# Optimization experiments

Measured on AMD Instinct MI355X. Metric: run time of the kernel, lower is better.

## Reference

```python
import jax, jax.numpy as jnp
import numpy as np

F, H, NSEQ, T, A, LP, LV = 256, 256, 64, 2048, 32, 512, 512
N = NSEQ * T


def setup_inputs() -> dict:
    key = jax.random.key(0)
    ks = jax.random.split(key, 24)
    p = lambda k, shape: jax.random.normal(k, shape, jnp.float32) * 0.05
    return {
        'features': jax.random.normal(ks[0], (N, F), jnp.float32),
        'episode_starts': (jax.random.uniform(ks[1], (N,)) < 0.005).astype(jnp.float32),
        'h_pi': jax.random.normal(ks[2], (1, NSEQ, H), jnp.float32),
        'c_pi': jax.random.normal(ks[3], (1, NSEQ, H), jnp.float32),
        'h_vf': jax.random.normal(ks[4], (1, NSEQ, H), jnp.float32),
        'c_vf': jax.random.normal(ks[5], (1, NSEQ, H), jnp.float32),
        'W_feat': p(ks[6], (4 * F, F)), 'b_feat': jnp.zeros((4 * F,), jnp.float32),
        'W_emb': p(ks[7], (H, F)), 'b_emb': jnp.zeros((H,), jnp.float32),
        'W_ih': p(ks[8], (4 * H, F)), 'W_hh': p(ks[9], (4 * H, H)),
        'b_ih': jnp.zeros((4 * H,), jnp.float32), 'b_hh': jnp.zeros((4 * H,), jnp.float32),
        'Wp1': p(ks[10], (LP, H + 3 * F)), 'bp1': jnp.zeros((LP,), jnp.float32),
        'Wp2': p(ks[11], (A, LP)), 'bp2': jnp.zeros((A,), jnp.float32),
        'Wv1': p(ks[12], (LV, H + 3 * F)), 'bv1': jnp.zeros((LV,), jnp.float32),
        'Wv2': p(ks[13], (1, LV)), 'bv2': jnp.zeros((1,), jnp.float32),
    }


def _lstm_masked_scan(feats, starts, h0, c0, W_ih, W_hh, b_ih, b_hh):
    # feats: (T, n_seq, F), starts: (T, n_seq); PyTorch gate order i,f,g,o
    xg = jnp.einsum('tnf,gf->tng', feats, W_ih) + b_ih  # precompute input gates

    def step(carry, xs):
        h, c = carry
        xg_t, s_t = xs
        m = (1.0 - s_t)[:, None]          # episode-reset mask
        h = h * m
        c = c * m
        g = xg_t + h @ W_hh.T + b_hh
        i, f, gg, o = jnp.split(g, 4, axis=-1)
        c = jax.nn.sigmoid(f) * c + jax.nn.sigmoid(i) * jnp.tanh(gg)
        h = jax.nn.sigmoid(o) * jnp.tanh(c)
        return (h, c), h

    (hT, cT), hs = jax.lax.scan(step, (h0, c0), (xg, starts))
    return hs, hT, cT


def reference(features, episode_starts, h_pi, c_pi, h_vf, c_vf,
              W_feat, b_feat, W_emb, b_emb, W_ih, W_hh, b_ih, b_hh,
              Wp1, bp1, Wp2, bp2, Wv1, bv1, Wv2, bv2):
    n_seq = h_vf.shape[1]
    feats = features.reshape(n_seq, -1, F).swapaxes(0, 1)      # (T, n_seq, F)
    starts = episode_starts.reshape(n_seq, -1).swapaxes(0, 1)  # (T, n_seq)

    feat4 = jnp.einsum('tnf,gf->tng', feats, W_feat) + b_feat  # (T, n_seq, 4F)
    f1 = feat4[..., : 3 * F]
    f1_flat = f1.swapaxes(0, 1).reshape(-1, 3 * F)             # (N, 3F)

    # actor branch: TempLSTM ignores its LSTM -> just Linear(F, H) on raw feats;
    # the loop branch feeds raw features_sequence (source behavior).
    out_pi = jnp.einsum('tnf,hf->tnh', feats, W_emb) + b_emb   # (T, n_seq, H)
    out_pi_flat = out_pi.swapaxes(0, 1).reshape(-1, H)

    # critic branch: masked LSTM recurrence with per-step episode resets
    hs, hT, cT = _lstm_masked_scan(feats, starts, h_vf[0], c_vf[0], W_ih, W_hh, b_ih, b_hh)
    hs_flat = hs.swapaxes(0, 1).reshape(-1, H)

    latent_pi = jnp.concatenate([f1_flat, out_pi_flat], axis=-1)
    latent_vf = jnp.concatenate([f1_flat, hs_flat], axis=-1)

    values = jax.nn.relu(latent_vf @ Wv1.T + bv1) @ Wv2.T + bv2      # (N, 1)
    logits = jax.nn.relu(latent_pi @ Wp1.T + bp1) @ Wp2.T + bp2      # (N, A)

    actions = jnp.argmax(logits, axis=-1)  # deterministic=True -> mode
    log_prob = jnp.take_along_axis(jax.nn.log_softmax(logits, axis=-1), actions[:, None], axis=1)[:, 0]

    # actor final state = h0 scaled by product of reset masks (loop semantics)
    mprod = jnp.prod(1.0 - starts, axis=0)[None, :, None]
    h_pi_f, c_pi_f = h_pi * mprod, c_pi * mprod
    return actions, values, log_prob, h_pi_f, c_pi_f, hT[None], cT[None]
```

## Files before the change

kernel.cpp:

```cpp
#include <hip/hip_runtime.h>
#include <stdint.h>
#include <math.h>

#define N_TOT 131072
#define TSEQ  2048
#define NSEQ  64
#define CS    128
#define NCH   16
#define PARTS 4

typedef unsigned long long u64;

__global__ __launch_bounds__(256)
void transpose_whh(const float* __restrict__ Whh, float* __restrict__ Wg)
{
    const int k = blockIdx.x;
    const int u = threadIdx.x;
#pragma unroll
    for (int g = 0; g < 4; ++g)
        Wg[(size_t)k * 1024 + u * 4 + g] = Whh[(size_t)(g * 256 + u) * 256 + k];
}

__global__ __launch_bounds__(256)
void gemm_xg(const float* __restrict__ A, const float* __restrict__ Wih,
             const float* __restrict__ bih, const float* __restrict__ bhh,
             float* __restrict__ xg, int base)
{
    __shared__ float As[16][136];
    __shared__ float Bs[16][136];
    const int t  = threadIdx.x;
    const int n0 = blockIdx.x * 128;
    const int seq = blockIdx.y;
    const size_t grow0 = (size_t)seq * TSEQ + base;
    const size_t lrow0 = (size_t)seq * CS;
    const int tx = t & 15, ty = t >> 4;

    float acc[8][8];
#pragma unroll
    for (int i = 0; i < 8; ++i)
#pragma unroll
        for (int j = 0; j < 8; ++j) acc[i][j] = 0.f;

    for (int kt = 0; kt < 256; kt += 16) {
#pragma unroll
        for (int jj = 0; jj < 2; ++jj) {
            int idx = t + 256 * jj;
            int m = idx >> 2, q = idx & 3;
            float4 a = *(const float4*)(A + (grow0 + m) * 256 + kt + q * 4);
            As[q * 4 + 0][m] = a.x; As[q * 4 + 1][m] = a.y;
            As[q * 4 + 2][m] = a.z; As[q * 4 + 3][m] = a.w;
            float4 b = *(const float4*)(Wih + (size_t)(n0 + m) * 256 + kt + q * 4);
            Bs[q * 4 + 0][m] = b.x; Bs[q * 4 + 1][m] = b.y;
            Bs[q * 4 + 2][m] = b.z; Bs[q * 4 + 3][m] = b.w;
        }
        __syncthreads();
#pragma unroll
        for (int k = 0; k < 16; ++k) {
            float4 a0 = *(const float4*)&As[k][ty * 8];
            float4 a1 = *(const float4*)&As[k][ty * 8 + 4];
            float4 b0 = *(const float4*)&Bs[k][tx * 8];
            float4 b1 = *(const float4*)&Bs[k][tx * 8 + 4];
            float av[8] = {a0.x, a0.y, a0.z, a0.w, a1.x, a1.y, a1.z, a1.w};
            float bv[8] = {b0.x, b0.y, b0.z, b0.w, b1.x, b1.y, b1.z, b1.w};
#pragma unroll
            for (int i = 0; i < 8; ++i)
#pragma unroll
                for (int j = 0; j < 8; ++j) acc[i][j] += av[i] * bv[j];
        }
        __syncthreads();
    }
#pragma unroll
    for (int i = 0; i < 8; ++i) {
        size_t lr = lrow0 + ty * 8 + i;
#pragma unroll
        for (int j = 0; j < 8; ++j) {
            int n = n0 + tx * 8 + j;
            int gate = n >> 8, u = n & 255;
            xg[lr * 1024 + u * 4 + gate] = acc[i][j] + bih[n] + bhh[n];
        }
    }
}

__device__ __forceinline__ void l2_store_u64(u64* p, u64 v)
{
    asm volatile("global_store_dwordx2 %0, %1, off"
                 :: "v"(p), "v"(v) : "memory");
}

__device__ __forceinline__ u64 l2_load_u64(const u64* p)
{
    u64 v;
    asm volatile("global_load_dwordx2 %0, %1, off sc0\n\t"
                 "s_waitcnt vmcnt(0)"
                 : "=v"(v) : "v"(p) : "memory");
    return v;
}

__global__ __launch_bounds__(1024)
void lstm4_h1p(const float* __restrict__ xg, const float* __restrict__ starts,
               const float* __restrict__ h0g, const float* __restrict__ c0g,
               float* __restrict__ hstate, float* __restrict__ cstate,
               const float* __restrict__ Wg,
               float* __restrict__ hs, float* __restrict__ hT,
               float* __restrict__ cT,
               u64* __restrict__ hx, u64* __restrict__ hx2,
               unsigned* __restrict__ fastState,
               const float* __restrict__ lat, const float* __restrict__ Wp1,
               const float* __restrict__ bp1, float* __restrict__ h1,
               int base, int fastflag)
{
    __shared__ float smem[9216];

    const int t   = threadIdx.x;
    const int bid = blockIdx.x;

    if (bid < 256) {
        float* hmask = smem;
        float* part  = smem + 256;

        const int slot = bid >> 3;
        const int seq  = (bid & 7) + 8 * (slot >> 2);
        const int p    = slot & 3;
        const int u    = t & 63;
        const int q    = t >> 6;

        float4 Wr[16];
#pragma unroll
        for (int kk = 0; kk < 16; ++kk)
            Wr[kk] = *(const float4*)(Wg + (size_t)(q * 16 + kk) * 1024 + (p * 64 + u) * 4);

        float c_reg = 0.f;
        if (t < 64) {
            const float* csrc = (base == 0) ? c0g : cstate;
            c_reg = csrc[(size_t)seq * 256 + p * 64 + t];
        }

        bool useFast = (fastflag != 0);
        if (useFast) {
            unsigned st = __hip_atomic_load(fastState, __ATOMIC_RELAXED,
                                            __HIP_MEMORY_SCOPE_AGENT);
            if (st != 0u) useFast = false;
        }

        for (int lt = 0; lt < CS; ++lt) {
            const int S = base + lt;
            const float m = 1.f - starts[(size_t)seq * TSEQ + S];

            float4 x4 = make_float4(0.f, 0.f, 0.f, 0.f);
            if (t < 64)
                x4 = *(const float4*)(xg + ((size_t)seq * CS + lt) * 1024 + (p * 64 + t) * 4);

            if (lt == 0) {
                if (t < 256) {
                    const float* hsrc = (base == 0) ? h0g : hstate;
                    hmask[t] = hsrc[(size_t)seq * 256 + t] * m;
                }
            } else {
                if (t < 256) {
                    const size_t idx = (size_t)(S & 1) * (NSEQ * 256) + (size_t)seq * 256 + t;
                    u64 w = 0;
                    if (useFast) {
                        int tries = 0;
                        for (;;) {
                            w = l2_load_u64(&hx2[idx]);
                            if ((unsigned)(w >> 32) == (unsigned)S) break;
                            if (++tries > 768) {
                                useFast = false;
                                __hip_atomic_store(fastState, 1u, __ATOMIC_RELAXED,
                                                   __HIP_MEMORY_SCOPE_AGENT);
                                break;
                            }
                        }
                    }
                    if (!useFast) {
                        unsigned spins = 0;
                        for (;;) {
                            w = __hip_atomic_load(&hx[idx], __ATOMIC_RELAXED,
                                                  __HIP_MEMORY_SCOPE_AGENT);
                            if ((unsigned)(w >> 32) == (unsigned)S) break;
                            __builtin_amdgcn_s_sleep(1);
                            if (++spins > (1u << 18)) break;
                        }
                    }
                    hmask[t] = __uint_as_float((unsigned)w) * m;
                }
            }
            __syncthreads();

            const float* hp = &hmask[q * 16];
            float4 h0 = *(const float4*)(hp + 0);
            float4 h1v_ = *(const float4*)(hp + 4);
            float4 h2 = *(const float4*)(hp + 8);
            float4 h3 = *(const float4*)(hp + 12);
            float hv[16] = {h0.x,h0.y,h0.z,h0.w, h1v_.x,h1v_.y,h1v_.z,h1v_.w,
                            h2.x,h2.y,h2.z,h2.w, h3.x,h3.y,h3.z,h3.w};
            float a0 = 0.f, a1 = 0.f, a2 = 0.f, a3 = 0.f;
#pragma unroll
            for (int kk = 0; kk < 16; ++kk) {
                a0 += hv[kk] * Wr[kk].x;
                a1 += hv[kk] * Wr[kk].y;
                a2 += hv[kk] * Wr[kk].z;
                a3 += hv[kk] * Wr[kk].w;
            }
            *(float4*)&part[(q * 64 + u) * 4] = make_float4(a0, a1, a2, a3);
            __syncthreads();

            if (t < 64) {
                float gi = 0.f, gf = 0.f, gg = 0.f, go = 0.f;
#pragma unroll
                for (int qq = 0; qq < 16; ++qq) {
                    float4 pp = *(const float4*)&part[(qq * 64 + t) * 4];
                    gi += pp.x; gf += pp.y; gg += pp.z; go += pp.w;
                }
                gi += x4.x; gf += x4.y; gg += x4.z; go += x4.w;
                float c = c_reg * m;
                float si = 1.f / (1.f + expf(-gi));
                float sf = 1.f / (1.f + expf(-gf));
                float so = 1.f / (1.f + expf(-go));
                c = sf * c + si * tanhf(gg);
                float h = so * tanhf(c);
                c_reg = c;

                const int gu = p * 64 + t;
                const size_t widx = (size_t)((S + 1) & 1) * (NSEQ * 256)
                                  + (size_t)seq * 256 + gu;
                const u64 pkt = ((u64)(unsigned)(S + 1) << 32)
                              | (u64)__float_as_uint(h);
                if (fastflag) l2_store_u64(&hx2[widx], pkt);
                __hip_atomic_store(&hx[widx], pkt,
                                   __ATOMIC_RELAXED, __HIP_MEMORY_SCOPE_AGENT);
                hs[((size_t)seq * CS + lt) * 256 + gu] = h;
                if (lt == CS - 1) {
                    cstate[(size_t)seq * 256 + gu] = c;
                    hstate[(size_t)seq * 256 + gu] = h;
                }
                if (S == TSEQ - 1) {
                    cT[(size_t)seq * 256 + gu] = c;
                    hT[(size_t)seq * 256 + gu] = h;
                }
            }
        }
    } else {
        const int s    = t >> 8;
        const int t2   = t & 255;
        const int tile = (bid - 256) * 4 + s;
        const int n0   = (tile & 7) * 64;
        const size_t lr0 = (size_t)(tile >> 3) * 64;
        float* As = smem + s * 2304;
        float* Bs = As + 1152;
        const int tx = t2 & 15, ty = t2 >> 4;

        double acc[4][4];
#pragma unroll
        for (int i = 0; i < 4; ++i)
#pragma unroll
            for (int j = 0; j < 4; ++j) acc[i][j] = 0.0;

        for (int kt = 0; kt < 1024; kt += 16) {
            {
                int m = t2 >> 2, q = t2 & 3;
                float4 a = *(const float4*)(lat + (lr0 + m) * 1024 + kt + q * 4);
                As[(q * 4 + 0) * 72 + m] = a.x; As[(q * 4 + 1) * 72 + m] = a.y;
                As[(q * 4 + 2) * 72 + m] = a.z; As[(q * 4 + 3) * 72 + m] = a.w;
                float4 b = *(const float4*)(Wp1 + (size_t)(n0 + m) * 1024 + kt + q * 4);
                Bs[(q * 4 + 0) * 72 + m] = b.x; Bs[(q * 4 + 1) * 72 + m] = b.y;
                Bs[(q * 4 + 2) * 72 + m] = b.z; Bs[(q * 4 + 3) * 72 + m] = b.w;
            }
            __syncthreads();
            float p[4][4];
#pragma unroll
            for (int i = 0; i < 4; ++i)
#pragma unroll
                for (int j = 0; j < 4; ++j) p[i][j] = 0.f;
#pragma unroll
            for (int k = 0; k < 16; ++k) {
                float4 a0 = *(const float4*)&As[k * 72 + ty * 4];
                float4 b0 = *(const float4*)&Bs[k * 72 + tx * 4];
                float av[4] = {a0.x, a0.y, a0.z, a0.w};
                float bv[4] = {b0.x, b0.y, b0.z, b0.w};
#pragma unroll
                for (int i = 0; i < 4; ++i)
#pragma unroll
                    for (int j = 0; j < 4; ++j) p[i][j] += av[i] * bv[j];
            }
#pragma unroll
            for (int i = 0; i < 4; ++i)
#pragma unroll
                for (int j = 0; j < 4; ++j) acc[i][j] += (double)p[i][j];
            __syncthreads();
        }
#pragma unroll
        for (int i = 0; i < 4; ++i) {
            size_t lr = lr0 + ty * 4 + i;
#pragma unroll
            for (int j = 0; j < 4; ++j) {
                int n = n0 + tx * 4 + j;
                float v = (float)acc[i][j] + bp1[n];
                h1[lr * 512 + n] = v > 0.f ? v : 0.f;
            }
        }
    }
}

__global__ __launch_bounds__(256)
void gemm_latent(const float* __restrict__ A, const float* __restrict__ Wfeat,
                 const float* __restrict__ Wemb, const float* __restrict__ bfeat,
                 const float* __restrict__ bemb, float* __restrict__ lat, int base)
{
    __shared__ float As[16][136];
    __shared__ float Bs[16][136];
    const int t  = threadIdx.x;
    const int n0 = blockIdx.x * 128;
    const size_t lr0 = (size_t)blockIdx.y * 128;
    const size_t grow0 = (lr0 >> 7) * TSEQ + base;
    const int tx = t & 15, ty = t >> 4;

    double acc[8][8];
#pragma unroll
    for (int i = 0; i < 8; ++i)
#pragma unroll
        for (int j = 0; j < 8; ++j) acc[i][j] = 0.0;

    for (int kt = 0; kt < 256; kt += 16) {
#pragma unroll
        for (int jj = 0; jj < 2; ++jj) {
            int idx = t + 256 * jj;
            int m = idx >> 2, q = idx & 3;
            float4 a = *(const float4*)(A + (grow0 + m) * 256 + kt + q * 4);
            As[q * 4 + 0][m] = a.x; As[q * 4 + 1][m] = a.y;
            As[q * 4 + 2][m] = a.z; As[q * 4 + 3][m] = a.w;
            int n = n0 + m;
            const float* Brow = (n < 768) ? (Wfeat + (size_t)n * 256)
                                          : (Wemb + (size_t)(n - 768) * 256);
            float4 b = *(const float4*)(Brow + kt + q * 4);
            Bs[q * 4 + 0][m] = b.x; Bs[q * 4 + 1][m] = b.y;
            Bs[q * 4 + 2][m] = b.z; Bs[q * 4 + 3][m] = b.w;
        }
        __syncthreads();
        float p[8][8];
#pragma unroll
        for (int i = 0; i < 8; ++i)
#pragma unroll
            for (int j = 0; j < 8; ++j) p[i][j] = 0.f;
#pragma unroll
        for (int k = 0; k < 16; ++k) {
            float4 a0 = *(const float4*)&As[k][ty * 8];
            float4 a1 = *(const float4*)&As[k][ty * 8 + 4];
            float4 b0 = *(const float4*)&Bs[k][tx * 8];
            float4 b1 = *(const float4*)&Bs[k][tx * 8 + 4];
            float av[8] = {a0.x, a0.y, a0.z, a0.w, a1.x, a1.y, a1.z, a1.w};
            float bv[8] = {b0.x, b0.y, b0.z, b0.w, b1.x, b1.y, b1.z, b1.w};
#pragma unroll
            for (int i = 0; i < 8; ++i)
#pragma unroll
                for (int j = 0; j < 8; ++j) p[i][j] += av[i] * bv[j];
        }
#pragma unroll
        for (int i = 0; i < 8; ++i)
#pragma unroll
            for (int j = 0; j < 8; ++j) acc[i][j] += (double)p[i][j];
        __syncthreads();
    }
#pragma unroll
    for (int i = 0; i < 8; ++i) {
        size_t lr = lr0 + ty * 8 + i;
#pragma unroll
        for (int j = 0; j < 8; ++j) {
            int n = n0 + tx * 8 + j;
            float v = (float)acc[i][j];
            v += (n < 768) ? bfeat[n] : bemb[n - 768];
            lat[lr * 1024 + n] = v;
        }
    }
}

__global__ __launch_bounds__(256)
void gemm_h1v(const float* __restrict__ lat, const float* __restrict__ hs,
              const float* __restrict__ Wv1, const float* __restrict__ bv1,
              float* __restrict__ h1)
{
    __shared__ float As[16][136];
    __shared__ float Bs[16][136];
    const int t  = threadIdx.x;
    const int n0 = blockIdx.x * 128;
    const size_t lrow0 = (size_t)blockIdx.y * 128;
    const int tx = t & 15, ty = t >> 4;

    float acc[8][8];
#pragma unroll
    for (int i = 0; i < 8; ++i)
#pragma unroll
        for (int j = 0; j < 8; ++j) acc[i][j] = 0.f;

    for (int pass = 0; pass < 2; ++pass) {
        const float* A  = (pass == 0) ? lat : hs;
        const int lda   = (pass == 0) ? 1024 : 256;
        const int kmax  = (pass == 0) ? 768 : 256;
        const int boff  = (pass == 0) ? 0 : 768;
        for (int kt = 0; kt < kmax; kt += 16) {
#pragma unroll
            for (int jj = 0; jj < 2; ++jj) {
                int idx = t + 256 * jj;
                int m = idx >> 2, q = idx & 3;
                float4 a = *(const float4*)(A + (lrow0 + m) * lda + kt + q * 4);
                As[q * 4 + 0][m] = a.x; As[q * 4 + 1][m] = a.y;
                As[q * 4 + 2][m] = a.z; As[q * 4 + 3][m] = a.w;
                float4 b = *(const float4*)(Wv1 + (size_t)(n0 + m) * 1024 + boff + kt + q * 4);
                Bs[q * 4 + 0][m] = b.x; Bs[q * 4 + 1][m] = b.y;
                Bs[q * 4 + 2][m] = b.z; Bs[q * 4 + 3][m] = b.w;
            }
            __syncthreads();
#pragma unroll
            for (int k = 0; k < 16; ++k) {
                float4 a0 = *(const float4*)&As[k][ty * 8];
                float4 a1 = *(const float4*)&As[k][ty * 8 + 4];
                float4 b0 = *(const float4*)&Bs[k][tx * 8];
                float4 b1 = *(const float4*)&Bs[k][tx * 8 + 4];
                float av[8] = {a0.x, a0.y, a0.z, a0.w, a1.x, a1.y, a1.z, a1.w};
                float bv[8] = {b0.x, b0.y, b0.z, b0.w, b1.x, b1.y, b1.z, b1.w};
#pragma unroll
                for (int i = 0; i < 8; ++i)
#pragma unroll
                    for (int j = 0; j < 8; ++j) acc[i][j] += av[i] * bv[j];
            }
            __syncthreads();
        }
    }
#pragma unroll
    for (int i = 0; i < 8; ++i) {
        size_t lr = lrow0 + ty * 8 + i;
#pragma unroll
        for (int j = 0; j < 8; ++j) {
            int n = n0 + tx * 8 + j;
            float v = acc[i][j] + bv1[n];
            h1[lr * 512 + n] = v > 0.f ? v : 0.f;
        }
    }
}

__global__ __launch_bounds__(256)
void mask_kernel(const float* __restrict__ starts, const float* __restrict__ h_pi,
                 const float* __restrict__ c_pi,
                 float* __restrict__ o_hpi, float* __restrict__ o_cpi)
{
    __shared__ float red[256];
    const int n = blockIdx.x, t = threadIdx.x;
    float a = 0.f;
    for (int j = 0; j < 8; ++j)
        a = fmaxf(a, starts[(size_t)n * TSEQ + t * 8 + j]);
    red[t] = a; __syncthreads();
    for (int s = 128; s > 0; s >>= 1) {
        if (t < s) red[t] = fmaxf(red[t], red[t + s]);
        __syncthreads();
    }
    float m = (red[0] > 0.f) ? 0.f : 1.f;
    o_hpi[(size_t)n * 256 + t] = h_pi[(size_t)n * 256 + t] * m;
    o_cpi[(size_t)n * 256 + t] = c_pi[(size_t)n * 256 + t] * m;
}

__global__ __launch_bounds__(256)
void policy_finish(const float* __restrict__ h1p, const float* __restrict__ Wp2,
                   const float* __restrict__ bp2,
                   float* __restrict__ o_actions, float* __restrict__ o_logp,
                   int base)
{
    __shared__ float w2t[512 * 32];
    const int t = threadIdx.x;
    for (int j = 0; j < 64; ++j) {
        int idx = t + 256 * j;
        int k = idx >> 5, c = idx & 31;
        w2t[idx] = Wp2[(size_t)c * 512 + k];
    }
    __syncthreads();

    const int c = t & 31;
    size_t lr = (size_t)blockIdx.x * 8 + (t >> 5);
    size_t grow = (lr >> 7) * TSEQ + base + (lr & 127);
    const float* hrow = h1p + lr * 512;
    double s = 0.0;
    for (int k = 0; k < 512; k += 4) {
        float4 h4 = *(const float4*)(hrow + k);
        s += (double)h4.x * (double)w2t[(k + 0) * 32 + c];
        s += (double)h4.y * (double)w2t[(k + 1) * 32 + c];
        s += (double)h4.z * (double)w2t[(k + 2) * 32 + c];
        s += (double)h4.w * (double)w2t[(k + 3) * 32 + c];
    }
    double logit = s + (double)bp2[c];

    double mv = logit; int mi = c;
#pragma unroll
    for (int off = 16; off >= 1; off >>= 1) {
        double ov = __shfl_xor(mv, off, 32);
        int    oi = __shfl_xor(mi, off, 32);
        if (ov > mv || (ov == mv && oi < mi)) { mv = ov; mi = oi; }
    }
    double se = exp(logit - mv);
#pragma unroll
    for (int off = 16; off >= 1; off >>= 1) se += __shfl_xor(se, off, 32);

    if (c == 0) {
        o_actions[grow] = (float)mi;
        o_logp[grow]    = (float)(-log(se));
    }
}

__global__ __launch_bounds__(256)
void value_finish(const float* __restrict__ h1v, const float* __restrict__ Wv2,
                  const float* __restrict__ bv2, float* __restrict__ o_values,
                  int base)
{
    __shared__ float wv[512];
    const int t = threadIdx.x;
    wv[t] = Wv2[t]; wv[t + 256] = Wv2[t + 256];
    __syncthreads();
    const int q = t & 3;
    size_t lr = (size_t)blockIdx.x * 64 + (t >> 2);
    size_t grow = (lr >> 7) * TSEQ + base + (lr & 127);
    const float* hrow = h1v + lr * 512;
    float s = 0.f;
    for (int k = q * 128; k < q * 128 + 128; k += 4) {
        float4 h4 = *(const float4*)(hrow + k);
        float4 w4 = *(const float4*)&wv[k];
        s += h4.x * w4.x + h4.y * w4.y + h4.z * w4.z + h4.w * w4.w;
    }
    s += __shfl_xor(s, 1, 4);
    s += __shfl_xor(s, 2, 4);
    if (q == 0) o_values[grow] = s + bv2[0];
}

extern "C" void kernel_launch(void* const* d_in, const int* in_sizes, int n_in,
                              void* d_out, int out_size, void* d_ws, size_t ws_size,
                              hipStream_t stream)
{
    const float* features = (const float*)d_in[0];
    const float* starts   = (const float*)d_in[1];
    const float* h_pi     = (const float*)d_in[2];
    const float* c_pi     = (const float*)d_in[3];
    const float* h_vf     = (const float*)d_in[4];
    const float* c_vf     = (const float*)d_in[5];
    const float* W_feat   = (const float*)d_in[6];
    const float* b_feat   = (const float*)d_in[7];
    const float* W_emb    = (const float*)d_in[8];
    const float* b_emb    = (const float*)d_in[9];
    const float* W_ih     = (const float*)d_in[10];
    const float* W_hh     = (const float*)d_in[11];
    const float* b_ih     = (const float*)d_in[12];
    const float* b_hh     = (const float*)d_in[13];
    const float* Wp1      = (const float*)d_in[14];
    const float* bp1      = (const float*)d_in[15];
    const float* Wp2      = (const float*)d_in[16];
    const float* bp2      = (const float*)d_in[17];
    const float* Wv1      = (const float*)d_in[18];
    const float* bv1      = (const float*)d_in[19];
    const float* Wv2      = (const float*)d_in[20];
    const float* bv2      = (const float*)d_in[21];

    float* out = (float*)d_out;
    float* o_actions = out;
    float* o_values  = out + N_TOT;
    float* o_logp    = out + 2 * (size_t)N_TOT;
    float* o_hpi     = out + 3 * (size_t)N_TOT;
    float* o_cpi     = o_hpi + NSEQ * 256;
    float* o_hT      = o_cpi + NSEQ * 256;
    float* o_cT      = o_hT  + NSEQ * 256;

    char* ws = (char*)d_ws;
    const size_t MB = 1024 * 1024;
    float* xg_c  = (float*)(ws);
    float* lat_c = (float*)(ws + 32 * MB);
    float* hs_c  = (float*)(ws + 64 * MB);
    float* h1_c  = (float*)(ws + 72 * MB);
    float* Wg    = (float*)(ws + 88 * MB);
    float* hstate = (float*)(ws + 89 * MB);
    float* cstate = (float*)(ws + 89 * MB + 65536);
    u64*   hx     = (u64*)  (ws + 89 * MB + 131072);
    u64*   hx2    = (u64*)  (ws + 89 * MB + 393216);
    unsigned* fastState = (unsigned*)(ws + 89 * MB + 655360);

    const int fastflag = (ws_size >= 89 * MB + 656 * 1024) ? 1 : 0;
    u64* hx2_eff = fastflag ? hx2 : hx;
    unsigned* fs_eff = fastflag ? fastState : (unsigned*)hx;

    transpose_whh<<<256, 256, 0, stream>>>(W_hh, Wg);

    mask_kernel<<<NSEQ, 256, 0, stream>>>(starts, h_pi, c_pi, o_hpi, o_cpi);

    for (int c = 0; c < NCH; ++c) {
        const int base = c * CS;

        gemm_xg<<<dim3(8, NSEQ), 256, 0, stream>>>(features, W_ih, b_ih, b_hh,
                                                   xg_c, base);
        gemm_latent<<<dim3(8, 64), 256, 0, stream>>>(
            features, W_feat, W_emb, b_feat, b_emb, lat_c, base);

        lstm4_h1p<<<512, 1024, 0, stream>>>(xg_c, starts, h_vf, c_vf,
                                            hstate, cstate, Wg,
                                            hs_c, o_hT, o_cT, hx, hx2_eff,
                                            fs_eff,
                                            lat_c, Wp1, bp1, h1_c,
                                            base, fastflag);

        policy_finish<<<1024, 256, 0, stream>>>(h1_c, Wp2, bp2,
                                                o_actions, o_logp, base);

        gemm_h1v<<<dim3(4, 64), 256, 0, stream>>>(lat_c, hs_c, Wv1, bv1, h1_c);
        value_finish<<<128, 256, 0, stream>>>(h1_c, Wv2, bv2, o_values, base);
    }
}
```

Before: 14.74 ms.

## Overlap next-chunk input GEMMs with LSTM recurrence using double-buffered chunks

Halves the chunk length to 64 timesteps and doubles the chunk count. The input-gate and latent GEMMs for the next chunk now run in extra blocks of the fused LSTM kernel, writing into double-buffered workspace, so the standalone pre-recurrence GEMM launches per chunk go away. The aim is to hide feature-projection work behind the latency-bound sequential recurrence and cut launch count per chunk. The cost is more chunks, and so more per-chunk launches of the finish kernels. The larger grid also risks co-residency problems for the spin-waiting recurrence blocks, and the value-path hidden buffer is aliased onto the current xg buffer.

```diff
diff --git a/kernel.cpp b/kernel.cpp
--- a/kernel.cpp
+++ b/kernel.cpp
@@ -5,8 +5,9 @@
 #define N_TOT 131072
 #define TSEQ  2048
 #define NSEQ  64
-#define CS    128
-#define NCH   16
+#define CS    64
+#define NCH   32
+#define ROWS  (NSEQ * CS)
 #define PARTS 4
 
 typedef unsigned long long u64;
@@ -19,66 +20,6 @@
 #pragma unroll
     for (int g = 0; g < 4; ++g)
         Wg[(size_t)k * 1024 + u * 4 + g] = Whh[(size_t)(g * 256 + u) * 256 + k];
-}
-
-__global__ __launch_bounds__(256)
-void gemm_xg(const float* __restrict__ A, const float* __restrict__ Wih,
-             const float* __restrict__ bih, const float* __restrict__ bhh,
-             float* __restrict__ xg, int base)
-{
-    __shared__ float As[16][136];
-    __shared__ float Bs[16][136];
-    const int t  = threadIdx.x;
-    const int n0 = blockIdx.x * 128;
-    const int seq = blockIdx.y;
-    const size_t grow0 = (size_t)seq * TSEQ + base;
-    const size_t lrow0 = (size_t)seq * CS;
-    const int tx = t & 15, ty = t >> 4;
-
-    float acc[8][8];
-#pragma unroll
-    for (int i = 0; i < 8; ++i)
-#pragma unroll
-        for (int j = 0; j < 8; ++j) acc[i][j] = 0.f;
-
-    for (int kt = 0; kt < 256; kt += 16) {
-#pragma unroll
-        for (int jj = 0; jj < 2; ++jj) {
-            int idx = t + 256 * jj;
-            int m = idx >> 2, q = idx & 3;
-            float4 a = *(const float4*)(A + (grow0 + m) * 256 + kt + q * 4);
-            As[q * 4 + 0][m] = a.x; As[q * 4 + 1][m] = a.y;
-            As[q * 4 + 2][m] = a.z; As[q * 4 + 3][m] = a.w;
-            float4 b = *(const float4*)(Wih + (size_t)(n0 + m) * 256 + kt + q * 4);
-            Bs[q * 4 + 0][m] = b.x; Bs[q * 4 + 1][m] = b.y;
-            Bs[q * 4 + 2][m] = b.z; Bs[q * 4 + 3][m] = b.w;
-        }
-        __syncthreads();
-#pragma unroll
-        for (int k = 0; k < 16; ++k) {
-            float4 a0 = *(const float4*)&As[k][ty * 8];
-            float4 a1 = *(const float4*)&As[k][ty * 8 + 4];
-            float4 b0 = *(const float4*)&Bs[k][tx * 8];
-            float4 b1 = *(const float4*)&Bs[k][tx * 8 + 4];
-            float av[8] = {a0.x, a0.y, a0.z, a0.w, a1.x, a1.y, a1.z, a1.w};
-            float bv[8] = {b0.x, b0.y, b0.z, b0.w, b1.x, b1.y, b1.z, b1.w};
-#pragma unroll
-            for (int i = 0; i < 8; ++i)
-#pragma unroll
-                for (int j = 0; j < 8; ++j) acc[i][j] += av[i] * bv[j];
-        }
-        __syncthreads();
-    }
-#pragma unroll
-    for (int i = 0; i < 8; ++i) {
-        size_t lr = lrow0 + ty * 8 + i;
-#pragma unroll
-        for (int j = 0; j < 8; ++j) {
-            int n = n0 + tx * 8 + j;
-            int gate = n >> 8, u = n & 255;
-            xg[lr * 1024 + u * 4 + gate] = acc[i][j] + bih[n] + bhh[n];
-        }
-    }
 }
 
 __device__ __forceinline__ void l2_store_u64(u64* p, u64 v)
@@ -96,18 +37,136 @@
     return v;
 }
 
-__global__ __launch_bounds__(1024)
-void lstm4_h1p(const float* __restrict__ xg, const float* __restrict__ starts,
-               const float* __restrict__ h0g, const float* __restrict__ c0g,
-               float* __restrict__ hstate, float* __restrict__ cstate,
-               const float* __restrict__ Wg,
-               float* __restrict__ hs, float* __restrict__ hT,
-               float* __restrict__ cT,
-               u64* __restrict__ hx, u64* __restrict__ hx2,
-               unsigned* __restrict__ fastState,
-               const float* __restrict__ lat, const float* __restrict__ Wp1,
-               const float* __restrict__ bp1, float* __restrict__ h1,
-               int base, int fastflag)
+__global__ __launch_bounds__(256)
+void gemm_feat(const float* __restrict__ feats,
+               const float* __restrict__ Wih, const float* __restrict__ bih,
+               const float* __restrict__ bhh, float* __restrict__ xgout,
+               const float* __restrict__ Wfeat, const float* __restrict__ Wemb,
+               const float* __restrict__ bfeat, const float* __restrict__ bemb,
+               float* __restrict__ latout, int base)
+{
+    __shared__ float As[1152];
+    __shared__ float Bs[1152];
+    const int t   = threadIdx.x;
+    const int bid = blockIdx.x;
+    const bool isXg = bid < 1024;
+    const int tile = isXg ? bid : bid - 1024;
+    const int n0   = (tile & 15) * 64;
+    const int seq  = tile >> 4;
+    const size_t grow0 = (size_t)seq * TSEQ + base;
+    const size_t lr0   = (size_t)seq * CS;
+    const int tx = t & 15, ty = t >> 4;
+
+    if (isXg) {
+        float acc[4][4];
+#pragma unroll
+        for (int i = 0; i < 4; ++i)
+#pragma unroll
+            for (int j = 0; j < 4; ++j) acc[i][j] = 0.f;
+        for (int kt = 0; kt < 256; kt += 16) {
+            int m = t >> 2, q = t & 3;
+            float4 a = *(const float4*)(feats + (grow0 + m) * 256 + kt + q * 4);
+            As[(q*4+0)*72+m]=a.x; As[(q*4+1)*72+m]=a.y;
+            As[(q*4+2)*72+m]=a.z; As[(q*4+3)*72+m]=a.w;
+            float4 b = *(const float4*)(Wih + (size_t)(n0 + m) * 256 + kt + q * 4);
+            Bs[(q*4+0)*72+m]=b.x; Bs[(q*4+1)*72+m]=b.y;
+            Bs[(q*4+2)*72+m]=b.z; Bs[(q*4+3)*72+m]=b.w;
+            __syncthreads();
+#pragma unroll
+            for (int k = 0; k < 16; ++k) {
+                float4 a0 = *(const float4*)&As[k*72 + ty*4];
+                float4 b0 = *(const float4*)&Bs[k*72 + tx*4];
+                float av[4] = {a0.x,a0.y,a0.z,a0.w};
+                float bv[4] = {b0.x,b0.y,b0.z,b0.w};
+#pragma unroll
+                for (int i = 0; i < 4; ++i)
+#pragma unroll
+                    for (int j = 0; j < 4; ++j) acc[i][j] += av[i]*bv[j];
+            }
+            __syncthreads();
+        }
+#pragma unroll
+        for (int i = 0; i < 4; ++i) {
+            size_t lr = lr0 + ty*4 + i;
+#pragma unroll
+            for (int j = 0; j < 4; ++j) {
+                int n = n0 + tx*4 + j;
+                int gate = n >> 8, u = n & 255;
+                xgout[lr*1024 + u*4 + gate] = acc[i][j] + bih[n] + bhh[n];
+            }
+        }
+    } else {
+        double acc[4][4];
+#pragma unroll
+        for (int i = 0; i < 4; ++i)
+#pragma unroll
+            for (int j = 0; j < 4; ++j) acc[i][j] = 0.0;
+        for (int kt = 0; kt < 256; kt += 16) {
+            int m = t >> 2, q = t & 3;
+            float4 a = *(const float4*)(feats + (grow0 + m) * 256 + kt + q * 4);
+            As[(q*4+0)*72+m]=a.x; As[(q*4+1)*72+m]=a.y;
+            As[(q*4+2)*72+m]=a.z; As[(q*4+3)*72+m]=a.w;
+            int n = n0 + m;
+            const float* Brow = (n < 768) ? (Wfeat + (size_t)n * 256)
+                                          : (Wemb + (size_t)(n - 768) * 256);
+            float4 b = *(const float4*)(Brow + kt + q * 4);
+            Bs[(q*4+0)*72+m]=b.x; Bs[(q*4+1)*72+m]=b.y;
+            Bs[(q*4+2)*72+m]=b.z; Bs[(q*4+3)*72+m]=b.w;
+            __syncthreads();
+            float p[4][4];
+#pragma unroll
+            for (int i = 0; i < 4; ++i)
+#pragma unroll
+                for (int j = 0; j < 4; ++j) p[i][j] = 0.f;
+#pragma unroll
+            for (int k = 0; k < 16; ++k) {
+                float4 a0 = *(const float4*)&As[k*72 + ty*4];
+                float4 b0 = *(const float4*)&Bs[k*72 + tx*4];
+                float av[4] = {a0.x,a0.y,a0.z,a0.w};
+                float bv[4] = {b0.x,b0.y,b0.z,b0.w};
+#pragma unroll
+                for (int i = 0; i < 4; ++i)
+#pragma unroll
+                    for (int j = 0; j < 4; ++j) p[i][j] += av[i]*bv[j];
+            }
+#pragma unroll
+            for (int i = 0; i < 4; ++i)
+#pragma unroll
+                for (int j = 0; j < 4; ++j) acc[i][j] += (double)p[i][j];
+            __syncthreads();
+        }
+#pragma unroll
+        for (int i = 0; i < 4; ++i) {
+            size_t lr = lr0 + ty*4 + i;
+#pragma unroll
+            for (int j = 0; j < 4; ++j) {
+                int n = n0 + tx*4 + j;
+                float v = (float)acc[i][j];
+                v += (n < 768) ? bfeat[n] : bemb[n - 768];
+                latout[lr*1024 + n] = v;
+            }
+        }
+    }
+}
+
+__global__ __launch_bounds__(1024, 8)
+void fused(const float* __restrict__ xg, const float* __restrict__ starts,
+           const float* __restrict__ h0g, const float* __restrict__ c0g,
+           float* __restrict__ hstate, float* __restrict__ cstate,
+           const float* __restrict__ Wg,
+           float* __restrict__ hs, float* __restrict__ hT,
+           float* __restrict__ cT,
+           u64* __restrict__ hx, u64* __restrict__ hx2,
+           unsigned* __restrict__ fastState,
+           const float* __restrict__ lat, const float* __restrict__ Wp1,
+           const float* __restrict__ bp1, float* __restrict__ h1,
+           const float* __restrict__ feats,
+           const float* __restrict__ Wih, const float* __restrict__ bih,
+           const float* __restrict__ bhh, float* __restrict__ xg_next,
+           const float* __restrict__ Wfeat, const float* __restrict__ Wemb,
+           const float* __restrict__ bfeat, const float* __restrict__ bemb,
+           float* __restrict__ lat_next,
+           int base, int fastflag, int doNext)
 {
     __shared__ float smem[9216];
 
@@ -189,10 +248,10 @@
 
             const float* hp = &hmask[q * 16];
             float4 h0 = *(const float4*)(hp + 0);
-            float4 h1v_ = *(const float4*)(hp + 4);
+            float4 h1f = *(const float4*)(hp + 4);
             float4 h2 = *(const float4*)(hp + 8);
             float4 h3 = *(const float4*)(hp + 12);
-            float hv[16] = {h0.x,h0.y,h0.z,h0.w, h1v_.x,h1v_.y,h1v_.z,h1v_.w,
+            float hv[16] = {h0.x,h0.y,h0.z,h0.w, h1f.x,h1f.y,h1f.z,h1f.w,
                             h2.x,h2.y,h2.z,h2.w, h3.x,h3.y,h3.z,h3.w};
             float a0 = 0.f, a1 = 0.f, a2 = 0.f, a3 = 0.f;
 #pragma unroll
@@ -240,7 +299,7 @@
                 }
             }
         }
-    } else {
+    } else if (bid < 384) {
         const int s    = t >> 8;
         const int t2   = t & 255;
         const int tile = (bid - 256) * 4 + s;
@@ -260,11 +319,11 @@
             {
                 int m = t2 >> 2, q = t2 & 3;
                 float4 a = *(const float4*)(lat + (lr0 + m) * 1024 + kt + q * 4);
-                As[(q * 4 + 0) * 72 + m] = a.x; As[(q * 4 + 1) * 72 + m] = a.y;
-                As[(q * 4 + 2) * 72 + m] = a.z; As[(q * 4 + 3) * 72 + m] = a.w;
+                As[(q*4+0)*72+m]=a.x; As[(q*4+1)*72+m]=a.y;
+                As[(q*4+2)*72+m]=a.z; As[(q*4+3)*72+m]=a.w;
                 float4 b = *(const float4*)(Wp1 + (size_t)(n0 + m) * 1024 + kt + q * 4);
-                Bs[(q * 4 + 0) * 72 + m] = b.x; Bs[(q * 4 + 1) * 72 + m] = b.y;
-                Bs[(q * 4 + 2) * 72 + m] = b.z; Bs[(q * 4 + 3) * 72 + m] = b.w;
+                Bs[(q*4+0)*72+m]=b.x; Bs[(q*4+1)*72+m]=b.y;
+                Bs[(q*4+2)*72+m]=b.z; Bs[(q*4+3)*72+m]=b.w;
             }
             __syncthreads();
             float p[4][4];
@@ -274,14 +333,14 @@
                 for (int j = 0; j < 4; ++j) p[i][j] = 0.f;
 #pragma unroll
             for (int k = 0; k < 16; ++k) {
-                float4 a0 = *(const float4*)&As[k * 72 + ty * 4];
-                float4 b0 = *(const float4*)&Bs[k * 72 + tx * 4];
-                float av[4] = {a0.x, a0.y, a0.z, a0.w};
-                float bv[4] = {b0.x, b0.y, b0.z, b0.w};
+                float4 a0 = *(const float4*)&As[k*72 + ty*4];
+                float4 b0 = *(const float4*)&Bs[k*72 + tx*4];
+                float av[4] = {a0.x,a0.y,a0.z,a0.w};
+                float bv[4] = {b0.x,b0.y,b0.z,b0.w};
 #pragma unroll
                 for (int i = 0; i < 4; ++i)
 #pragma unroll
-                    for (int j = 0; j < 4; ++j) p[i][j] += av[i] * bv[j];
+                    for (int j = 0; j < 4; ++j) p[i][j] += av[i]*bv[j];
             }
 #pragma unroll
             for (int i = 0; i < 4; ++i)
@@ -291,85 +350,132 @@
         }
 #pragma unroll
         for (int i = 0; i < 4; ++i) {
-            size_t lr = lr0 + ty * 4 + i;
+            size_t lr = lr0 + ty*4 + i;
 #pragma unroll
             for (int j = 0; j < 4; ++j) {
-                int n = n0 + tx * 4 + j;
+                int n = n0 + tx*4 + j;
                 float v = (float)acc[i][j] + bp1[n];
                 h1[lr * 512 + n] = v > 0.f ? v : 0.f;
             }
         }
-    }
-}
-
-__global__ __launch_bounds__(256)
-void gemm_latent(const float* __restrict__ A, const float* __restrict__ Wfeat,
-                 const float* __restrict__ Wemb, const float* __restrict__ bfeat,
-                 const float* __restrict__ bemb, float* __restrict__ lat, int base)
-{
-    __shared__ float As[16][136];
-    __shared__ float Bs[16][136];
-    const int t  = threadIdx.x;
-    const int n0 = blockIdx.x * 128;
-    const size_t lr0 = (size_t)blockIdx.y * 128;
-    const size_t grow0 = (lr0 >> 7) * TSEQ + base;
-    const int tx = t & 15, ty = t >> 4;
-
-    double acc[8][8];
-#pragma unroll
-    for (int i = 0; i < 8; ++i)
-#pragma unroll
-        for (int j = 0; j < 8; ++j) acc[i][j] = 0.0;
-
-    for (int kt = 0; kt < 256; kt += 16) {
-#pragma unroll
-        for (int jj = 0; jj < 2; ++jj) {
-            int idx = t + 256 * jj;
-            int m = idx >> 2, q = idx & 3;
-            float4 a = *(const float4*)(A + (grow0 + m) * 256 + kt + q * 4);
-            As[q * 4 + 0][m] = a.x; As[q * 4 + 1][m] = a.y;
-            As[q * 4 + 2][m] = a.z; As[q * 4 + 3][m] = a.w;
-            int n = n0 + m;
-            const float* Brow = (n < 768) ? (Wfeat + (size_t)n * 256)
-                                          : (Wemb + (size_t)(n - 768) * 256);
-            float4 b = *(const float4*)(Brow + kt + q * 4);
-            Bs[q * 4 + 0][m] = b.x; Bs[q * 4 + 1][m] = b.y;
-            Bs[q * 4 + 2][m] = b.z; Bs[q * 4 + 3][m] = b.w;
-        }
-        __syncthreads();
-        float p[8][8];
-#pragma unroll
-        for (int i = 0; i < 8; ++i)
-#pragma unroll
-            for (int j = 0; j < 8; ++j) p[i][j] = 0.f;
-#pragma unroll
-        for (int k = 0; k < 16; ++k) {
-            float4 a0 = *(const float4*)&As[k][ty * 8];
-            float4 a1 = *(const float4*)&As[k][ty * 8 + 4];
-            float4 b0 = *(const float4*)&Bs[k][tx * 8];
-            float4 b1 = *(const float4*)&Bs[k][tx * 8 + 4];
-            float av[8] = {a0.x, a0.y, a0.z, a0.w, a1.x, a1.y, a1.z, a1.w};
-            float bv[8] = {b0.x, b0.y, b0.z, b0.w, b1.x, b1.y, b1.z, b1.w};
-#pragma unroll
-            for (int i = 0; i < 8; ++i)
-#pragma unroll
-                for (int j = 0; j < 8; ++j) p[i][j] += av[i] * bv[j];
-        }
-#pragma unroll
-        for (int i = 0; i < 8; ++i)
-#pragma unroll
-            for (int j = 0; j < 8; ++j) acc[i][j] += (double)p[i][j];
-        __syncthreads();
-    }
-#pragma unroll
-    for (int i = 0; i < 8; ++i) {
-        size_t lr = lr0 + ty * 8 + i;
-#pragma unroll
-        for (int j = 0; j < 8; ++j) {
-            int n = n0 + tx * 8 + j;
-            float v = (float)acc[i][j];
-            v += (n < 768) ? bfeat[n] : bemb[n - 768];
-            lat[lr * 1024 + n] = v;
+    } else if (bid < 640) {
+        if (!doNext) return;
+        const int s    = t >> 8;
+        const int t2   = t & 255;
+        const int tile = (bid - 384) * 4 + s;
+        const int n0   = (tile & 15) * 64;
+        const int seq  = tile >> 4;
+        const size_t grow0 = (size_t)seq * TSEQ + base + CS;
+        const size_t lr0   = (size_t)seq * CS;
+        float* As = smem + s * 2304;
+        float* Bs = As + 1152;
+        const int tx = t2 & 15, ty = t2 >> 4;
+
+        float acc[4][4];
+#pragma unroll
+        for (int i = 0; i < 4; ++i)
+#pragma unroll
+            for (int j = 0; j < 4; ++j) acc[i][j] = 0.f;
+
+        for (int kt = 0; kt < 256; kt += 16) {
+            {
+                int m = t2 >> 2, q = t2 & 3;
+                float4 a = *(const float4*)(feats + (grow0 + m) * 256 + kt + q * 4);
+                As[(q*4+0)*72+m]=a.x; As[(q*4+1)*72+m]=a.y;
+                As[(q*4+2)*72+m]=a.z; As[(q*4+3)*72+m]=a.w;
+                float4 b = *(const float4*)(Wih + (size_t)(n0 + m) * 256 + kt + q * 4);
+                Bs[(q*4+0)*72+m]=b.x; Bs[(q*4+1)*72+m]=b.y;
+                Bs[(q*4+2)*72+m]=b.z; Bs[(q*4+3)*72+m]=b.w;
+            }
+            __syncthreads();
+#pragma unroll
+            for (int k = 0; k < 16; ++k) {
+                float4 a0 = *(const float4*)&As[k*72 + ty*4];
+                float4 b0 = *(const float4*)&Bs[k*72 + tx*4];
+                float av[4] = {a0.x,a0.y,a0.z,a0.w};
+                float bv[4] = {b0.x,b0.y,b0.z,b0.w};
+#pragma unroll
+                for (int i = 0; i < 4; ++i)
+#pragma unroll
+                    for (int j = 0; j < 4; ++j) acc[i][j] += av[i]*bv[j];
+            }
+            __syncthreads();
+        }
+#pragma unroll
+        for (int i = 0; i < 4; ++i) {
+            size_t lr = lr0 + ty*4 + i;
+#pragma unroll
+            for (int j = 0; j < 4; ++j) {
+                int n = n0 + tx*4 + j;
+                int gate = n >> 8, u = n & 255;
+                xg_next[lr*1024 + u*4 + gate] = acc[i][j] + bih[n] + bhh[n];
+            }
+        }
+    } else {
+        if (!doNext) return;
+        const int s    = t >> 8;
+        const int t2   = t & 255;
+        const int tile = (bid - 640) * 4 + s;
+        const int n0   = (tile & 15) * 64;
+        const int seq  = tile >> 4;
+        const size_t grow0 = (size_t)seq * TSEQ + base + CS;
+        const size_t lr0   = (size_t)seq * CS;
+        float* As = smem + s * 2304;
+        float* Bs = As + 1152;
+        const int tx = t2 & 15, ty = t2 >> 4;
+
+        double acc[4][4];
+#pragma unroll
+        for (int i = 0; i < 4; ++i)
+#pragma unroll
+            for (int j = 0; j < 4; ++j) acc[i][j] = 0.0;
+
+        for (int kt = 0; kt < 256; kt += 16) {
+            {
+                int m = t2 >> 2, q = t2 & 3;
+                float4 a = *(const float4*)(feats + (grow0 + m) * 256 + kt + q * 4);
+                As[(q*4+0)*72+m]=a.x; As[(q*4+1)*72+m]=a.y;
+                As[(q*4+2)*72+m]=a.z; As[(q*4+3)*72+m]=a.w;
+                int n = n0 + m;
+                const float* Brow = (n < 768) ? (Wfeat + (size_t)n * 256)
+                                              : (Wemb + (size_t)(n - 768) * 256);
+                float4 b = *(const float4*)(Brow + kt + q * 4);
+                Bs[(q*4+0)*72+m]=b.x; Bs[(q*4+1)*72+m]=b.y;
+                Bs[(q*4+2)*72+m]=b.z; Bs[(q*4+3)*72+m]=b.w;
+            }
+            __syncthreads();
+            float p[4][4];
+#pragma unroll
+            for (int i = 0; i < 4; ++i)
+#pragma unroll
+                for (int j = 0; j < 4; ++j) p[i][j] = 0.f;
+#pragma unroll
+            for (int k = 0; k < 16; ++k) {
+                float4 a0 = *(const float4*)&As[k*72 + ty*4];
+                float4 b0 = *(const float4*)&Bs[k*72 + tx*4];
+                float av[4] = {a0.x,a0.y,a0.z,a0.w};
+                float bv[4] = {b0.x,b0.y,b0.z,b0.w};
+#pragma unroll
+                for (int i = 0; i < 4; ++i)
+#pragma unroll
+                    for (int j = 0; j < 4; ++j) p[i][j] += av[i]*bv[j];
+            }
+#pragma unroll
+            for (int i = 0; i < 4; ++i)
+#pragma unroll
+                for (int j = 0; j < 4; ++j) acc[i][j] += (double)p[i][j];
+            __syncthreads();
+        }
+#pragma unroll
+        for (int i = 0; i < 4; ++i) {
+            size_t lr = lr0 + ty*4 + i;
+#pragma unroll
+            for (int j = 0; j < 4; ++j) {
+                int n = n0 + tx*4 + j;
+                float v = (float)acc[i][j];
+                v += (n < 768) ? bfeat[n] : bemb[n - 768];
+                lat_next[lr*1024 + n] = v;
+            }
         }
     }
 }
@@ -377,7 +483,7 @@
 __global__ __launch_bounds__(256)
 void gemm_h1v(const float* __restrict__ lat, const float* __restrict__ hs,
               const float* __restrict__ Wv1, const float* __restrict__ bv1,
-              float* __restrict__ h1)
+              float* __restrict__ h1out)
 {
     __shared__ float As[16][136];
     __shared__ float Bs[16][136];
@@ -433,7 +539,7 @@
         for (int j = 0; j < 8; ++j) {
             int n = n0 + tx * 8 + j;
             float v = acc[i][j] + bv1[n];
-            h1[lr * 512 + n] = v > 0.f ? v : 0.f;
+            h1out[lr * 512 + n] = v > 0.f ? v : 0.f;
         }
     }
 }
@@ -474,33 +580,36 @@
     __syncthreads();
 
     const int c = t & 31;
-    size_t lr = (size_t)blockIdx.x * 8 + (t >> 5);
-    size_t grow = (lr >> 7) * TSEQ + base + (lr & 127);
-    const float* hrow = h1p + lr * 512;
-    double s = 0.0;
-    for (int k = 0; k < 512; k += 4) {
-        float4 h4 = *(const float4*)(hrow + k);
-        s += (double)h4.x * (double)w2t[(k + 0) * 32 + c];
-        s += (double)h4.y * (double)w2t[(k + 1) * 32 + c];
-        s += (double)h4.z * (double)w2t[(k + 2) * 32 + c];
-        s += (double)h4.w * (double)w2t[(k + 3) * 32 + c];
-    }
-    double logit = s + (double)bp2[c];
-
-    double mv = logit; int mi = c;
-#pragma unroll
-    for (int off = 16; off >= 1; off >>= 1) {
-        double ov = __shfl_xor(mv, off, 32);
-        int    oi = __shfl_xor(mi, off, 32);
-        if (ov > mv || (ov == mv && oi < mi)) { mv = ov; mi = oi; }
-    }
-    double se = exp(logit - mv);
-#pragma unroll
-    for (int off = 16; off >= 1; off >>= 1) se += __shfl_xor(se, off, 32);
-
-    if (c == 0) {
-        o_actions[grow] = (float)mi;
-        o_logp[grow]    = (float)(-log(se));
+    const int g = t >> 5;
+    for (int it = 0; it < 4; ++it) {
+        size_t lr = (size_t)blockIdx.x * 32 + it * 8 + g;
+        size_t grow = (lr >> 6) * TSEQ + base + (lr & 63);
+        const float* hrow = h1p + lr * 512;
+        double s = 0.0;
+        for (int k = 0; k < 512; k += 4) {
+            float4 h4 = *(const float4*)(hrow + k);
+            s += (double)h4.x * (double)w2t[(k + 0) * 32 + c];
+            s += (double)h4.y * (double)w2t[(k + 1) * 32 + c];
+            s += (double)h4.z * (double)w2t[(k + 2) * 32 + c];
+            s += (double)h4.w * (double)w2t[(k + 3) * 32 + c];
+        }
+        double logit = s + (double)bp2[c];
+
+        double mv = logit; int mi = c;
+#pragma unroll
+        for (int off = 16; off >= 1; off >>= 1) {
+            double ov = __shfl_xor(mv, off, 32);
+            int    oi = __shfl_xor(mi, off, 32);
+            if (ov > mv || (ov == mv && oi < mi)) { mv = ov; mi = oi; }
+        }
+        double se = exp(logit - mv);
+#pragma unroll
+        for (int off = 16; off >= 1; off >>= 1) se += __shfl_xor(se, off, 32);
+
+        if (c == 0) {
+            o_actions[grow] = (float)mi;
+            o_logp[grow]    = (float)(-log(se));
+        }
     }
 }
 
@@ -515,7 +624,7 @@
     __syncthreads();
     const int q = t & 3;
     size_t lr = (size_t)blockIdx.x * 64 + (t >> 2);
-    size_t grow = (lr >> 7) * TSEQ + base + (lr & 127);
+    size_t grow = (lr >> 6) * TSEQ + base + (lr & 63);
     const float* hrow = h1v + lr * 512;
     float s = 0.f;
     for (int k = q * 128; k < q * 128 + 128; k += 4) {
@@ -566,44 +675,48 @@
 
     char* ws = (char*)d_ws;
     const size_t MB = 1024 * 1024;
-    float* xg_c  = (float*)(ws);
-    float* lat_c = (float*)(ws + 32 * MB);
+    float* xg0   = (float*)(ws);
+    float* xg1   = (float*)(ws + 16 * MB);
+    float* lat0  = (float*)(ws + 32 * MB);
+    float* lat1  = (float*)(ws + 48 * MB);
     float* hs_c  = (float*)(ws + 64 * MB);
-    float* h1_c  = (float*)(ws + 72 * MB);
-    float* Wg    = (float*)(ws + 88 * MB);
-    float* hstate = (float*)(ws + 89 * MB);
-    float* cstate = (float*)(ws + 89 * MB + 65536);
-    u64*   hx     = (u64*)  (ws + 89 * MB + 131072);
-    u64*   hx2    = (u64*)  (ws + 89 * MB + 393216);
-    unsigned* fastState = (unsigned*)(ws + 89 * MB + 655360);
-
-    const int fastflag = (ws_size >= 89 * MB + 656 * 1024) ? 1 : 0;
-    u64* hx2_eff = fastflag ? hx2 : hx;
-    unsigned* fs_eff = fastflag ? fastState : (unsigned*)hx;
+    float* h1_c  = (float*)(ws + 68 * MB);
+    float* Wg    = (float*)(ws + 76 * MB);
+    float* hstate = (float*)(ws + 77 * MB);
+    float* cstate = (float*)(ws + 77 * MB + 65536);
+    u64*   hx     = (u64*)  (ws + 77 * MB + 131072);
+    u64*   hx2    = (u64*)  (ws + 77 * MB + 393216);
+    unsigned* fastState = (unsigned*)(ws + 77 * MB + 655360);
+
+    const int fastflag = (ws_size >= 78 * MB) ? 1 : 0;
 
     transpose_whh<<<256, 256, 0, stream>>>(W_hh, Wg);
-
     mask_kernel<<<NSEQ, 256, 0, stream>>>(starts, h_pi, c_pi, o_hpi, o_cpi);
+
+    gemm_feat<<<2048, 256, 0, stream>>>(features, W_ih, b_ih, b_hh, xg0,
+                                        W_feat, W_emb, b_feat, b_emb, lat0, 0);
 
     for (int c = 0; c < NCH; ++c) {
         const int base = c * CS;
-
-        gemm_xg<<<dim3(8, NSEQ), 256, 0, stream>>>(features, W_ih, b_ih, b_hh,
-                                                   xg_c, base);
-        gemm_latent<<<dim3(8, 64), 256, 0, stream>>>(
-            features, W_feat, W_emb, b_feat, b_emb, lat_c, base);
-
-        lstm4_h1p<<<512, 1024, 0, stream>>>(xg_c, starts, h_vf, c_vf,
-                                            hstate, cstate, Wg,
-                                            hs_c, o_hT, o_cT, hx, hx2_eff,
-                                            fs_eff,
-                                            lat_c, Wp1, bp1, h1_c,
-                                            base, fastflag);
-
-        policy_finish<<<1024, 256, 0, stream>>>(h1_c, Wp2, bp2,
-                                                o_actions, o_logp, base);
-
-        gemm_h1v<<<dim3(4, 64), 256, 0, stream>>>(lat_c, hs_c, Wv1, bv1, h1_c);
-        value_finish<<<128, 256, 0, stream>>>(h1_c, Wv2, bv2, o_values, base);
-    }
-}
+        float* xg_cur  = (c & 1) ? xg1 : xg0;
+        float* xg_nxt  = (c & 1) ? xg0 : xg1;
+        float* lat_cur = (c & 1) ? lat1 : lat0;
+        float* lat_nxt = (c & 1) ? lat0 : lat1;
+        const int doNext = (c < NCH - 1) ? 1 : 0;
+
+        fused<<<896, 1024, 0, stream>>>(xg_cur, starts, h_vf, c_vf,
+                                        hstate, cstate, Wg,
+                                        hs_c, o_hT, o_cT, hx, hx2, fastState,
+                                        lat_cur, Wp1, bp1, h1_c,
+                                        features, W_ih, b_ih, b_hh, xg_nxt,
+                                        W_feat, W_emb, b_feat, b_emb, lat_nxt,
+                                        base, fastflag, doNext);
+
+        policy_finish<<<128, 256, 0, stream>>>(h1_c, Wp2, bp2,
+                                               o_actions, o_logp, base);
+
+        gemm_h1v<<<dim3(4, 32), 256, 0, stream>>>(lat_cur, hs_c, Wv1, bv1,
+                                                  xg_cur);
+        value_finish<<<64, 256, 0, stream>>>(xg_cur, Wv2, bv2, o_values, base);
+    }
+}
```

New measurement: 35.82 ms. +143.0%, slower.
